# Kernel optimization log

Measured on AMD Instinct MI355X. Metric: run time of the kernel, lower is better.

Reference implementation:

```python
import jax, jax.numpy as jnp
import numpy as np

N_NODES = 50000
N_EDGES = 1600000
N_GRAPHS = 512
HEADS = 4
HEAD_DIM = 32
LAYERS = 3
NEG_SLOPE = 0.2


def setup_inputs() -> dict:
    key = jax.random.key(0)
    ks = jax.random.split(key, 7)
    x = jax.random.normal(ks[0], (N_NODES, 128), dtype=jnp.float32)
    Ws = jax.random.normal(ks[1], (LAYERS, 128, 128), dtype=jnp.float32) * 0.1
    att_src = jax.random.normal(ks[2], (LAYERS, HEADS, HEAD_DIM), dtype=jnp.float32) * 0.1
    att_dst = jax.random.normal(ks[3], (LAYERS, HEADS, HEAD_DIM), dtype=jnp.float32) * 0.1
    biases = jnp.zeros((LAYERS, 128), dtype=jnp.float32)
    edge_index = jax.random.randint(ks[4], (2, N_EDGES), 0, N_NODES, dtype=jnp.int64)
    batch = jnp.sort(jax.random.randint(ks[5], (N_NODES,), 0, N_GRAPHS, dtype=jnp.int64))
    return {"x": x, "Ws": Ws, "att_src": att_src, "att_dst": att_dst,
            "biases": biases, "edge_index": edge_index, "batch": batch}


def _gat_layer(x, W, a_s, a_d, b, src, dst, n):
    # linear transform -> per-head features [N, H, C]
    h = (x @ W).reshape(n, HEADS, HEAD_DIM)
    # per-node attention halves [N, H]
    alpha_src = jnp.einsum('nhc,hc->nh', h, a_s)
    alpha_dst = jnp.einsum('nhc,hc->nh', h, a_d)
    # edge logits [E, H]
    e = jax.nn.leaky_relu(alpha_src[src] + alpha_dst[dst], NEG_SLOPE)
    # segment softmax over incoming edges of each destination node
    m = jax.ops.segment_max(e, dst, num_segments=n)
    w = jnp.exp(e - m[dst])
    denom = jax.ops.segment_sum(w, dst, num_segments=n)
    alpha = w / (denom[dst] + 1e-16)
    # weighted scatter-add of source features [E, H, C] -> [N, H, C]
    msg = h[src] * alpha[:, :, None]
    out = jax.ops.segment_sum(msg, dst, num_segments=n)
    return out.reshape(n, HEADS * HEAD_DIM) + b


def reference(x, Ws, att_src, att_dst, biases, edge_index, batch):
    n = x.shape[0]
    # PyG GATConv adds self-loops by default
    loops = jnp.arange(n, dtype=edge_index.dtype)
    src = jnp.concatenate([edge_index[0], loops])
    dst = jnp.concatenate([edge_index[1], loops])
    for l in range(LAYERS):
        x = jax.nn.elu(_gat_layer(x, Ws[l], att_src[l], att_dst[l], biases[l], src, dst, n))
        # dropout is identity in eval mode
    # global mean pool over graphs
    sums = jax.ops.segment_sum(x, batch, num_segments=N_GRAPHS)
    cnt = jax.ops.segment_sum(jnp.ones((n,), x.dtype), batch, num_segments=N_GRAPHS)
    return sums / jnp.maximum(cnt, 1.0)[:, None]
```

## Files before the change

kernel.cpp:

```cpp
#include <hip/hip_runtime.h>
#include <hip/hip_fp16.h>
#include <math.h>

#define HEADS 4
#define HDIM 32
#define FD 128
#define NEG 0.2f
#define BCAP 4608
#define CH 8192
#define CHW 128

typedef _Float16 f16x8 __attribute__((ext_vector_type(8)));
typedef float f32x4 __attribute__((ext_vector_type(4)));

__device__ __forceinline__ float lrelu(float x) { return fmaxf(x, NEG * x); }

__global__ __launch_bounds__(256) void k_prepW(const float* __restrict__ W,
                                               const float* __restrict__ att_s,
                                               const float* __restrict__ att_d,
                                               _Float16* __restrict__ W16T,
                                               float* __restrict__ va_s,
                                               float* __restrict__ va_d) {
    int l = blockIdx.x;
    const float* Wl = W + (long)l * FD * FD;
    _Float16* o = W16T + (long)l * FD * FD;
    for (int i = threadIdx.x; i < FD * FD; i += 256) {
        int k = i >> 7, n = i & 127;
        o[n * FD + k] = (_Float16)Wl[i];
    }
    const float* as_l = att_s + l * HEADS * HDIM;
    const float* ad_l = att_d + l * HEADS * HDIM;
    for (int idx = threadIdx.x; idx < HEADS * FD; idx += 256) {
        int hd = idx >> 7, k = idx & 127;
        float ss = 0.f, dd = 0.f;
        for (int c = 0; c < HDIM; ++c) {
            float w = Wl[k * FD + hd * HDIM + c];
            ss += w * as_l[hd * HDIM + c];
            dd += w * ad_l[hd * HDIM + c];
        }
        va_s[(long)l * HEADS * FD + idx] = ss;
        va_d[(long)l * HEADS * FD + idx] = dd;
    }
}

__global__ __launch_bounds__(256) void k_cvt(const float* __restrict__ x,
                                             __half* __restrict__ o, long n) {
    long i = ((long)blockIdx.x * 256 + threadIdx.x) * 4;
    if (i < n) {
        float4 v = *(const float4*)&x[i];
        *(__half2*)&o[i] = __floats2half2_rn(v.x, v.y);
        *(__half2*)&o[i + 2] = __floats2half2_rn(v.z, v.w);
    }
}

__global__ __launch_bounds__(256) void k_gemm_mfma(const __half* __restrict__ x16,
                                                   const _Float16* __restrict__ W16T,
                                                   __half* __restrict__ h, int N) {
    __shared__ _Float16 wl[FD * FD];
    int t = threadIdx.x;
    for (int i = t * 8; i < FD * FD; i += 2048)
        *(f16x8*)&wl[i] = *(const f16x8*)&W16T[i];

    int w = t >> 6, lane = t & 63;
    int m = lane & 15, quad = lane >> 4;
    int row0 = blockIdx.x * 128 + w * 32;

    f16x8 a[2][4];
    f16x8 zf = {};
#pragma unroll
    for (int rt = 0; rt < 2; ++rt) {
        int gr = row0 + rt * 16 + m;
#pragma unroll
        for (int kc = 0; kc < 4; ++kc)
            a[rt][kc] = (gr < N) ? *(const f16x8*)&x16[(long)gr * FD + kc * 32 + quad * 8] : zf;
    }
    f32x4 acc[2][8];
#pragma unroll
    for (int rt = 0; rt < 2; ++rt)
#pragma unroll
        for (int c = 0; c < 8; ++c) acc[rt][c] = (f32x4){0.f, 0.f, 0.f, 0.f};

    __syncthreads();
#pragma unroll
    for (int c = 0; c < 8; ++c) {
        int nb = c * 16 + m;
#pragma unroll
        for (int kc = 0; kc < 4; ++kc) {
            f16x8 b = *(f16x8*)&wl[nb * FD + kc * 32 + quad * 8];
            acc[0][c] = __builtin_amdgcn_mfma_f32_16x16x32_f16(a[0][kc], b, acc[0][c], 0, 0, 0);
            acc[1][c] = __builtin_amdgcn_mfma_f32_16x16x32_f16(a[1][kc], b, acc[1][c], 0, 0, 0);
        }
    }
#pragma unroll
    for (int rt = 0; rt < 2; ++rt) {
        int rbase = row0 + rt * 16 + quad * 4;
#pragma unroll
        for (int c = 0; c < 8; ++c) {
            int col = c * 16 + m;
#pragma unroll
            for (int i = 0; i < 4; ++i) {
                int gr = rbase + i;
                if (gr < N) h[(long)gr * FD + col] = __float2half(acc[rt][c][i]);
            }
        }
    }
}

__global__ __launch_bounds__(256) void k_alpha(const __half* __restrict__ h,
                                               const float* __restrict__ a_s,
                                               const float* __restrict__ a_d,
                                               float* __restrict__ as_o,
                                               float* __restrict__ ad_o, int N) {
    int t = threadIdx.x;
    int n = blockIdx.x * 16 + (t >> 4);
    if (n >= N) return;
    int c16 = t & 15, gh = c16 >> 2, cb = c16 * 8;
    int c32 = (c16 & 3) * 8;
    float4 raw = *(const float4*)&h[(long)n * FD + cb];
    const __half* hh = (const __half*)&raw;
    float vs = 0.f, vd = 0.f;
#pragma unroll
    for (int i = 0; i < 8; ++i) {
        float hv = __half2float(hh[i]);
        vs += hv * a_s[gh * HDIM + c32 + i];
        vd += hv * a_d[gh * HDIM + c32 + i];
    }
    vs += __shfl_xor(vs, 1); vs += __shfl_xor(vs, 2);
    vd += __shfl_xor(vd, 1); vd += __shfl_xor(vd, 2);
    if ((c16 & 3) == 0) {
        as_o[n * HEADS + gh] = vs;
        ad_o[n * HEADS + gh] = vd;
    }
}

__global__ void k_zero_f(float* __restrict__ p, long n) {
    long i = (long)blockIdx.x * 256 + threadIdx.x;
    if (i < n) p[i] = 0.f;
}
__global__ void k_zero_i(int* __restrict__ p, int n) {
    int i = blockIdx.x * 256 + threadIdx.x;
    if (i < n) p[i] = 0;
}

__global__ __launch_bounds__(1024) void k_bin(const int* __restrict__ ei, int NE,
                                              int nbuck,
                                              int* __restrict__ bcnt,
                                              int* __restrict__ binned) {
    __shared__ int hist[512];
    __shared__ int gbase[512];
    int t = threadIdx.x;
    int c0 = blockIdx.x * CH;
    if (t < 512) hist[t] = 0;
    __syncthreads();
    int sub[8], val[8], loff[8];
#pragma unroll
    for (int k = 0; k < 8; ++k) {
        int idx = c0 + k * 1024 + t;
        sub[k] = -1;
        if (idx < NE) {
            int s = ei[idx], d = ei[NE + idx];
            sub[k] = d >> 7;
            val[k] = s | ((d & 127) << 16);
            loff[k] = atomicAdd(&hist[sub[k]], 1);
        }
    }
    __syncthreads();
    if (t < 512 && t < nbuck && hist[t] > 0)
        gbase[t] = atomicAdd(&bcnt[t], hist[t]);
    __syncthreads();
#pragma unroll
    for (int k = 0; k < 8; ++k) {
        if (sub[k] >= 0) {
            int p = gbase[sub[k]] + loff[k];
            if (p < BCAP) binned[(long)sub[k] * BCAP + p] = val[k];
        }
    }
}

__global__ __launch_bounds__(1024) void k_scan_sub(const int* __restrict__ bcnt,
                                                   int* __restrict__ bbase, int n,
                                                   int* __restrict__ rowstart, int N, int NE,
                                                   float* __restrict__ cnt, int G) {
    __shared__ int sm[1024];
    int t = threadIdx.x;
    if (t >= 512) {
        int i = t - 512;
        if (i < G) cnt[i] = 0.f;
    }
    int c0 = t * 4;
    int v0 = (c0 < n) ? bcnt[c0] : 0;
    int v1 = (c0 + 1 < n) ? bcnt[c0 + 1] : 0;
    int v2 = (c0 + 2 < n) ? bcnt[c0 + 2] : 0;
    int v3 = (c0 + 3 < n) ? bcnt[c0 + 3] : 0;
    int tot = v0 + v1 + v2 + v3;
    sm[t] = tot;
    __syncthreads();
    for (int off = 1; off < 1024; off <<= 1) {
        int u = (t >= off) ? sm[t - off] : 0;
        __syncthreads();
        sm[t] += u;
        __syncthreads();
    }
    int base = sm[t] - tot;
    if (c0 < n) bbase[c0] = base;
    if (c0 + 1 < n) bbase[c0 + 1] = base + v0;
    if (c0 + 2 < n) bbase[c0 + 2] = base + v0 + v1;
    if (c0 + 3 < n) bbase[c0 + 3] = base + v0 + v1 + v2;
    if (t == 1023) {
        bbase[n] = sm[1023];
        rowstart[N] = NE;
    }
}

__global__ __launch_bounds__(256) void k_bucket_csr(const int* __restrict__ binned,
                                                    const int* __restrict__ bcnt,
                                                    const int* __restrict__ bbase,
                                                    int* __restrict__ csr_src,
                                                    int* __restrict__ rowstart, int N) {
    int b = blockIdx.x;
    int t = threadIdx.x;
    __shared__ int ldeg[128], lofs[128], lcur[128];
    __shared__ int lcsr[BCAP];
    if (t < 128) ldeg[t] = 0;
    __syncthreads();
    int cnt = bcnt[b];
    if (cnt > BCAP) cnt = BCAP;
    int base = bbase[b];
    const int* reg = binned + (long)b * BCAP;
    for (int i = t; i < cnt; i += 256)
        atomicAdd(&ldeg[reg[i] >> 16], 1);
    __syncthreads();
    if (t < 128) lofs[t] = ldeg[t];
    __syncthreads();
    for (int off = 1; off < 128; off <<= 1) {
        int u = (t < 128 && t >= off) ? lofs[t - off] : 0;
        __syncthreads();
        if (t < 128) lofs[t] += u;
        __syncthreads();
    }
    if (t < 128) lcur[t] = lofs[t] - ldeg[t];
    __syncthreads();
    for (int i = t; i < cnt; i += 256) {
        int v = reg[i];
        int p = atomicAdd(&lcur[v >> 16], 1);
        lcsr[p] = v & 0xFFFF;
    }
    __syncthreads();
    for (int i = t; i < cnt; i += 256) csr_src[base + i] = lcsr[i];
    if (t < 128) {
        int d = b * 128 + t;
        if (d < N) rowstart[d] = base + lofs[t] - ldeg[t];
    }
}

__global__ __launch_bounds__(256) void k_aggr(const int* __restrict__ csr_src,
                                              const int* __restrict__ rowstart,
                                              const float* __restrict__ as_,
                                              const float* __restrict__ ad_,
                                              const __half* __restrict__ h,
                                              const float* __restrict__ bias,
                                              const float* __restrict__ va_s,
                                              const float* __restrict__ va_d,
                                              float* __restrict__ as_n,
                                              float* __restrict__ ad_n,
                                              __half* __restrict__ out, int N) {
    __shared__ int s_all[4][CHW];
    int t = threadIdx.x;
    int wv = t >> 6, lane = t & 63;
    int n = blockIdx.x * 4 + wv;
    if (n >= N) return;
    int* s_lds = s_all[wv];
    int c16 = lane & 15, rg = lane >> 4;
    int gh = c16 >> 2;
    int cb = c16 * 8;
    int beg = rowstart[n], end = rowstart[n + 1];
    int deg = end - beg;
    float adn = ad_[n * HEADS + gh];
    float l = 0.f;
    float acc[8] = {0.f, 0.f, 0.f, 0.f, 0.f, 0.f, 0.f, 0.f};

    for (int c0 = 0; c0 < deg; c0 += CHW) {
        int cnt = deg - c0;
        if (cnt > CHW) cnt = CHW;
        for (int i = lane; i < cnt; i += 64) s_lds[i] = csr_src[beg + c0 + i];
        __builtin_amdgcn_wave_barrier();
#pragma unroll 2
        for (int e = rg; e < cnt; e += 4) {
            int s = s_lds[e];
            float lg = lrelu(as_[s * HEADS + gh] + adn);
            float w = __expf(fminf(lg, 30.f));
            l += w;
            float4 raw = *(const float4*)&h[(long)s * FD + cb];
            const __half* hh = (const __half*)&raw;
#pragma unroll
            for (int i = 0; i < 8; ++i)
                acc[i] += __half2float(hh[i]) * w;
        }
        __builtin_amdgcn_wave_barrier();
    }
    l += __shfl_xor(l, 16);
    l += __shfl_xor(l, 32);
#pragma unroll
    for (int i = 0; i < 8; ++i) {
        acc[i] += __shfl_xor(acc[i], 16);
        acc[i] += __shfl_xor(acc[i], 32);
    }
    float sl = lrelu(as_[n * HEADS + gh] + adn);
    float sw = __expf(fminf(sl, 30.f));
    float inv = 1.f / (l + sw + 1e-16f);
    float4 rawh = *(const float4*)&h[(long)n * FD + cb];
    const __half* hh = (const __half*)&rawh;
    float4 b0 = *(const float4*)&bias[cb];
    float4 b1 = *(const float4*)&bias[cb + 4];
    float bb[8] = {b0.x, b0.y, b0.z, b0.w, b1.x, b1.y, b1.z, b1.w};
    float v[8];
#pragma unroll
    for (int i = 0; i < 8; ++i) {
        float u = (acc[i] + sw * __half2float(hh[i])) * inv + bb[i];
        v[i] = u > 0.f ? u : expm1f(u);
    }
    if (rg == 0) {
        __half o8[8];
#pragma unroll
        for (int i = 0; i < 8; ++i) o8[i] = __float2half(v[i]);
        *(float4*)&out[(long)n * FD + cb] = *(float4*)o8;
    }
    if (va_s) {
        const float* vs = va_s + rg * FD + cb;
        const float* vd = va_d + rg * FD + cb;
        float ps = 0.f, pd = 0.f;
#pragma unroll
        for (int i = 0; i < 8; ++i) {
            ps += v[i] * vs[i];
            pd += v[i] * vd[i];
        }
        for (int off = 1; off < 16; off <<= 1) {
            ps += __shfl_xor(ps, off);
            pd += __shfl_xor(pd, off);
        }
        if (c16 == 0) {
            as_n[n * HEADS + rg] = ps;
            ad_n[n * HEADS + rg] = pd;
        }
    }
}

__global__ __launch_bounds__(128) void k_pool(const __half* __restrict__ x,
                                              const int* __restrict__ batch,
                                              float* __restrict__ out,
                                              float* __restrict__ cnt, int N) {
    int n0 = blockIdx.x * 32;
    if (n0 >= N) return;
    int n1 = n0 + 32;
    if (n1 > N) n1 = N;
    int ch = threadIdx.x;
    __shared__ int gb[32];
    if (ch < n1 - n0) gb[ch] = batch[n0 + ch];
    __syncthreads();
    int g = gb[0];
    float sum = 0.f, c_local = 0.f;
    for (int n = n0; n < n1; ++n) {
        int gn = gb[n - n0];
        if (gn != g) {
            atomicAdd(&out[(long)g * FD + ch], sum);
            if (ch == 0) atomicAdd(&cnt[g], c_local);
            sum = 0.f;
            c_local = 0.f;
            g = gn;
        }
        sum += __half2float(x[(long)n * FD + ch]);
        c_local += 1.f;
    }
    atomicAdd(&out[(long)g * FD + ch], sum);
    if (ch == 0) atomicAdd(&cnt[g], c_local);
}

__global__ void k_div(float* __restrict__ out, const float* __restrict__ cnt, int G) {
    int i = blockIdx.x * 256 + threadIdx.x;
    if (i >= G * FD) return;
    float c = cnt[i >> 7];
    out[i] /= (c > 1.f ? c : 1.f);
}

extern "C" void kernel_launch(void* const* d_in, const int* in_sizes, int n_in,
                              void* d_out, int out_size, void* d_ws, size_t ws_size,
                              hipStream_t stream) {
    const float* x0     = (const float*)d_in[0];
    const float* Wall   = (const float*)d_in[1];
    const float* att_s  = (const float*)d_in[2];
    const float* att_d  = (const float*)d_in[3];
    const float* biases = (const float*)d_in[4];
    const int*   ei     = (const int*)d_in[5];
    const int*   batch  = (const int*)d_in[6];
    float*       out    = (float*)d_out;

    int N  = in_sizes[0] / FD;
    int NE = in_sizes[5] / 2;
    int G  = out_size / FD;

    int nbuck = (N + 127) >> 7;

    long nF = (long)N * FD;
    float*    wsf      = (float*)d_ws;
    float*    asA      = wsf;
    float*    adA      = asA + (long)N * HEADS;
    float*    asB      = adA + (long)N * HEADS;
    float*    adB      = asB + (long)N * HEADS;
    float*    cnt      = adB + (long)N * HEADS;
    float*    va_s     = cnt + G;
    float*    va_d     = va_s + 3 * HEADS * FD;
    int*      rowstart = (int*)(va_d + 3 * HEADS * FD);
    int*      bcnt     = rowstart + N + 1;
    int*      bbase    = bcnt + nbuck;
    int*      csr_src  = bbase + nbuck + 1;
    __half*   h        = (__half*)(csr_src + NE);
    __half*   x16      = h + nF;
    _Float16* W16T     = (_Float16*)(x16 + nF);
    int*      binned   = (int*)(W16T + 3 * FD * FD);

    k_zero_i<<<(nbuck + 255) / 256, 256, 0, stream>>>(bcnt, nbuck);
    k_bin<<<(NE + CH - 1) / CH, 1024, 0, stream>>>(ei, NE, nbuck, bcnt, binned);
    k_scan_sub<<<1, 1024, 0, stream>>>(bcnt, bbase, nbuck, rowstart, N, NE, cnt, G);
    k_bucket_csr<<<nbuck, 256, 0, stream>>>(binned, bcnt, bbase, csr_src, rowstart, N);
    k_prepW<<<3, 256, 0, stream>>>(Wall, att_s, att_d, W16T, va_s, va_d);
    k_cvt<<<(int)((nF / 4 + 255) / 256), 256, 0, stream>>>(x0, x16, nF);

    float* asR[3] = {asA, asB, asA};
    float* adR[3] = {adA, adB, adA};
    for (int l = 0; l < 3; ++l) {
        k_gemm_mfma<<<(N + 127) / 128, 256, 0, stream>>>(x16, W16T + (long)l * FD * FD, h, N);
        if (l == 0)
            k_alpha<<<(N + 15) / 16, 256, 0, stream>>>(h, att_s, att_d, asA, adA, N);
        const float* vs = (l < 2) ? va_s + (long)(l + 1) * HEADS * FD : nullptr;
        const float* vd = (l < 2) ? va_d + (long)(l + 1) * HEADS * FD : nullptr;
        k_aggr<<<(N + 3) / 4, 256, 0, stream>>>(csr_src, rowstart, asR[l], adR[l], h,
                                                biases + l * FD, vs, vd,
                                                asR[l + 1 < 3 ? l + 1 : 0],
                                                adR[l + 1 < 3 ? l + 1 : 0], x16, N);
    }

    k_zero_f<<<(G * FD + 255) / 256, 256, 0, stream>>>(out, G * FD);
    k_pool<<<(N + 31) / 32, 128, 0, stream>>>(x16, batch, out, cnt, N);
    k_div<<<(G * FD + 255) / 256, 256, 0, stream>>>(out, cnt, G);
}
```

Before: 362.1 us.

## Dedupe per-edge attention weights in aggregation and merge small setup kernels

In the aggregation kernel, each edge's softmax weight was previously computed redundantly by all 16 lanes sharing a head. It is now computed once per (edge, head) in a separate pass, stored in LDS, and read back during the feature accumulation, with the partial sums reduced across lanes. Separately, the weight-prep, fp32-to-fp16 conversion and bucket-count zeroing are merged into one launch, and the output zeroing moves into the scan kernel, cutting the launch count. The weight cache adds 8KB of LDS per block, which may reduce occupancy.

```diff
diff --git a/kernel.cpp b/kernel.cpp
--- a/kernel.cpp
+++ b/kernel.cpp
@@ -15,18 +15,36 @@
 
 __device__ __forceinline__ float lrelu(float x) { return fmaxf(x, NEG * x); }
 
-__global__ __launch_bounds__(256) void k_prepW(const float* __restrict__ W,
-                                               const float* __restrict__ att_s,
-                                               const float* __restrict__ att_d,
-                                               _Float16* __restrict__ W16T,
-                                               float* __restrict__ va_s,
-                                               float* __restrict__ va_d) {
-    int l = blockIdx.x;
+__global__ __launch_bounds__(256) void k_prep(const float* __restrict__ x,
+                                              __half* __restrict__ o, long nF,
+                                              const float* __restrict__ W,
+                                              const float* __restrict__ att_s,
+                                              const float* __restrict__ att_d,
+                                              _Float16* __restrict__ W16T,
+                                              float* __restrict__ va_s,
+                                              float* __restrict__ va_d,
+                                              int* __restrict__ bcnt, int nbuck,
+                                              int ncvt) {
+    int b = blockIdx.x;
+    if (b < ncvt) {
+        long i = ((long)b * 256 + threadIdx.x) * 4;
+        if (i < nF) {
+            float4 v = *(const float4*)&x[i];
+            *(__half2*)&o[i] = __floats2half2_rn(v.x, v.y);
+            *(__half2*)&o[i + 2] = __floats2half2_rn(v.z, v.w);
+        }
+        return;
+    }
+    if (b == ncvt + 3) {
+        for (int i = threadIdx.x; i < nbuck; i += 256) bcnt[i] = 0;
+        return;
+    }
+    int l = b - ncvt;
     const float* Wl = W + (long)l * FD * FD;
-    _Float16* o = W16T + (long)l * FD * FD;
+    _Float16* ow = W16T + (long)l * FD * FD;
     for (int i = threadIdx.x; i < FD * FD; i += 256) {
         int k = i >> 7, n = i & 127;
-        o[n * FD + k] = (_Float16)Wl[i];
+        ow[n * FD + k] = (_Float16)Wl[i];
     }
     const float* as_l = att_s + l * HEADS * HDIM;
     const float* ad_l = att_d + l * HEADS * HDIM;
@@ -43,16 +61,6 @@
     }
 }
 
-__global__ __launch_bounds__(256) void k_cvt(const float* __restrict__ x,
-                                             __half* __restrict__ o, long n) {
-    long i = ((long)blockIdx.x * 256 + threadIdx.x) * 4;
-    if (i < n) {
-        float4 v = *(const float4*)&x[i];
-        *(__half2*)&o[i] = __floats2half2_rn(v.x, v.y);
-        *(__half2*)&o[i + 2] = __floats2half2_rn(v.z, v.w);
-    }
-}
-
 __global__ __launch_bounds__(256) void k_gemm_mfma(const __half* __restrict__ x16,
                                                    const _Float16* __restrict__ W16T,
                                                    __half* __restrict__ h, int N) {
@@ -131,15 +139,6 @@
         as_o[n * HEADS + gh] = vs;
         ad_o[n * HEADS + gh] = vd;
     }
-}
-
-__global__ void k_zero_f(float* __restrict__ p, long n) {
-    long i = (long)blockIdx.x * 256 + threadIdx.x;
-    if (i < n) p[i] = 0.f;
-}
-__global__ void k_zero_i(int* __restrict__ p, int n) {
-    int i = blockIdx.x * 256 + threadIdx.x;
-    if (i < n) p[i] = 0;
 }
 
 __global__ __launch_bounds__(1024) void k_bin(const int* __restrict__ ei, int NE,
@@ -180,13 +179,10 @@
 __global__ __launch_bounds__(1024) void k_scan_sub(const int* __restrict__ bcnt,
                                                    int* __restrict__ bbase, int n,
                                                    int* __restrict__ rowstart, int N, int NE,
-                                                   float* __restrict__ cnt, int G) {
+                                                   float* __restrict__ cnt, int G,
+                                                   float* __restrict__ outz) {
     __shared__ int sm[1024];
     int t = threadIdx.x;
-    if (t >= 512) {
-        int i = t - 512;
-        if (i < G) cnt[i] = 0.f;
-    }
     int c0 = t * 4;
     int v0 = (c0 < n) ? bcnt[c0] : 0;
     int v1 = (c0 + 1 < n) ? bcnt[c0 + 1] : 0;
@@ -194,6 +190,7 @@
     int v3 = (c0 + 3 < n) ? bcnt[c0 + 3] : 0;
     int tot = v0 + v1 + v2 + v3;
     sm[t] = tot;
+    if (t < G) cnt[t] = 0.f;
     __syncthreads();
     for (int off = 1; off < 1024; off <<= 1) {
         int u = (t >= off) ? sm[t - off] : 0;
@@ -210,6 +207,9 @@
         bbase[n] = sm[1023];
         rowstart[N] = NE;
     }
+    long tot_out = (long)G * FD;
+    for (long i = t * 4; i < tot_out; i += 4096)
+        *(float4*)&outz[i] = (float4){0.f, 0.f, 0.f, 0.f};
 }
 
 __global__ __launch_bounds__(256) void k_bucket_csr(const int* __restrict__ binned,
@@ -265,17 +265,20 @@
                                               float* __restrict__ ad_n,
                                               __half* __restrict__ out, int N) {
     __shared__ int s_all[4][CHW];
+    __shared__ float w_all[4][CHW * 4];
     int t = threadIdx.x;
     int wv = t >> 6, lane = t & 63;
     int n = blockIdx.x * 4 + wv;
     if (n >= N) return;
     int* s_lds = s_all[wv];
+    float* w_lds = w_all[wv];
     int c16 = lane & 15, rg = lane >> 4;
     int gh = c16 >> 2;
     int cb = c16 * 8;
+    int we = lane >> 2, hd = lane & 3;
     int beg = rowstart[n], end = rowstart[n + 1];
     int deg = end - beg;
-    float adn = ad_[n * HEADS + gh];
+    float adn_w = ad_[n * HEADS + hd];
     float l = 0.f;
     float acc[8] = {0.f, 0.f, 0.f, 0.f, 0.f, 0.f, 0.f, 0.f};
 
@@ -284,12 +287,18 @@
         if (cnt > CHW) cnt = CHW;
         for (int i = lane; i < cnt; i += 64) s_lds[i] = csr_src[beg + c0 + i];
         __builtin_amdgcn_wave_barrier();
+        for (int e = we; e < cnt; e += 16) {
+            int s = s_lds[e];
+            float lg = lrelu(as_[s * HEADS + hd] + adn_w);
+            float w = __expf(fminf(lg, 30.f));
+            w_lds[e * 4 + hd] = w;
+            l += w;
+        }
+        __builtin_amdgcn_wave_barrier();
 #pragma unroll 2
         for (int e = rg; e < cnt; e += 4) {
             int s = s_lds[e];
-            float lg = lrelu(as_[s * HEADS + gh] + adn);
-            float w = __expf(fminf(lg, 30.f));
-            l += w;
+            float w = w_lds[e * 4 + gh];
             float4 raw = *(const float4*)&h[(long)s * FD + cb];
             const __half* hh = (const __half*)&raw;
 #pragma unroll
@@ -298,16 +307,20 @@
         }
         __builtin_amdgcn_wave_barrier();
     }
+    l += __shfl_xor(l, 4);
+    l += __shfl_xor(l, 8);
     l += __shfl_xor(l, 16);
     l += __shfl_xor(l, 32);
+    float l_gh = __shfl(l, gh);
 #pragma unroll
     for (int i = 0; i < 8; ++i) {
         acc[i] += __shfl_xor(acc[i], 16);
         acc[i] += __shfl_xor(acc[i], 32);
     }
-    float sl = lrelu(as_[n * HEADS + gh] + adn);
+    float adn_g = ad_[n * HEADS + gh];
+    float sl = lrelu(as_[n * HEADS + gh] + adn_g);
     float sw = __expf(fminf(sl, 30.f));
-    float inv = 1.f / (l + sw + 1e-16f);
+    float inv = 1.f / (l_gh + sw + 1e-16f);
     float4 rawh = *(const float4*)&h[(long)n * FD + cb];
     const __half* hh = (const __half*)&rawh;
     float4 b0 = *(const float4*)&bias[cb];
@@ -418,12 +431,13 @@
     _Float16* W16T     = (_Float16*)(x16 + nF);
     int*      binned   = (int*)(W16T + 3 * FD * FD);
 
-    k_zero_i<<<(nbuck + 255) / 256, 256, 0, stream>>>(bcnt, nbuck);
+    int ncvt = (int)((nF / 4 + 255) / 256);
+
+    k_prep<<<ncvt + 4, 256, 0, stream>>>(x0, x16, nF, Wall, att_s, att_d,
+                                         W16T, va_s, va_d, bcnt, nbuck, ncvt);
     k_bin<<<(NE + CH - 1) / CH, 1024, 0, stream>>>(ei, NE, nbuck, bcnt, binned);
-    k_scan_sub<<<1, 1024, 0, stream>>>(bcnt, bbase, nbuck, rowstart, N, NE, cnt, G);
+    k_scan_sub<<<1, 1024, 0, stream>>>(bcnt, bbase, nbuck, rowstart, N, NE, cnt, G, out);
     k_bucket_csr<<<nbuck, 256, 0, stream>>>(binned, bcnt, bbase, csr_src, rowstart, N);
-    k_prepW<<<3, 256, 0, stream>>>(Wall, att_s, att_d, W16T, va_s, va_d);
-    k_cvt<<<(int)((nF / 4 + 255) / 256), 256, 0, stream>>>(x0, x16, nF);
 
     float* asR[3] = {asA, asB, asA};
     float* adR[3] = {adA, adB, adA};
@@ -439,7 +453,6 @@
                                                 adR[l + 1 < 3 ? l + 1 : 0], x16, N);
     }
 
-    k_zero_f<<<(G * FD + 255) / 256, 256, 0, stream>>>(out, G * FD);
     k_pool<<<(N + 31) / 32, 128, 0, stream>>>(x16, batch, out, cnt, N);
     k_div<<<(G * FD + 255) / 256, 256, 0, stream>>>(out, cnt, G);
 }
```

Result: slower. 371.5 us (+2.6%).
